# Kernel tuning notes

Measured on AMD Instinct MI355X. Metric: run time of the kernel, lower is better.

The kernel has to match this reference:

```python
import jax, jax.numpy as jnp
import numpy as np

N_HEAD = 16


def setup_inputs() -> dict:
    key = jax.random.key(0)
    ks = jax.random.split(key, 9)
    B, T, C = 4, 2048, 1024
    s = 1.0 / np.sqrt(C)
    x = jax.random.normal(ks[0], (B, T, C), dtype=jnp.float32)
    Wq = jax.random.normal(ks[1], (C, C), dtype=jnp.float32) * s
    bq = jnp.zeros((C,), dtype=jnp.float32)
    Wk = jax.random.normal(ks[2], (C, C), dtype=jnp.float32) * s
    bk = jnp.zeros((C,), dtype=jnp.float32)
    Wv = jax.random.normal(ks[3], (C, C), dtype=jnp.float32) * s
    bv = jnp.zeros((C,), dtype=jnp.float32)
    Wp = jax.random.normal(ks[4], (C, C), dtype=jnp.float32) * s
    bp = jnp.zeros((C,), dtype=jnp.float32)
    return {"x": x, "Wq": Wq, "bq": bq, "Wk": Wk, "bk": bk,
            "Wv": Wv, "bv": bv, "Wp": Wp, "bp": bp}


def reference(x, Wq, bq, Wk, bk, Wv, bv, Wp, bp):
    B, T, C = x.shape
    H = N_HEAD
    D = C // H
    # QKV projections, then split heads: [B, T, C] -> [B, H, T, D]
    def split_heads(t):
        return t.reshape(B, T, H, D).transpose(0, 2, 1, 3)
    q = split_heads(x @ Wq.T + bq)
    k = split_heads(x @ Wk.T + bk)
    v = split_heads(x @ Wv.T + bv)
    # NOTE: original code applies NO causal mask despite the class name.
    att = jnp.einsum('bhtd,bhsd->bhts', q, k) * (1.0 / jnp.sqrt(jnp.float32(D)))
    att = jax.nn.softmax(att, axis=-1)
    y = jnp.einsum('bhts,bhsd->bhtd', att, v)  # [B, H, T, D]
    y = y.transpose(0, 2, 1, 3).reshape(B, T, C)
    return y @ Wp.T + bp
```

## Files before the change

kernel.cpp:

```cpp
#include <hip/hip_runtime.h>
#include <hip/hip_bf16.h>

typedef float  f32x4   __attribute__((ext_vector_type(4)));
typedef short  bf16x8  __attribute__((ext_vector_type(8)));

__device__ __forceinline__ ushort f2b(float f) {
  union { float f; unsigned u; } x; x.f = f;
  unsigned r = x.u + 0x7fffu + ((x.u >> 16) & 1u);
  return (ushort)(r >> 16);
}

__device__ __forceinline__ unsigned pkr(float lo, float hi) {
  unsigned lu = __float_as_uint(lo) + 0x8000u;
  unsigned hu = __float_as_uint(hi) + 0x8000u;
  return __builtin_amdgcn_perm(hu, lu, 0x07060302u);
}

__device__ __forceinline__ f32x4 fzero() {
  f32x4 z; z[0] = 0.f; z[1] = 0.f; z[2] = 0.f; z[3] = 0.f; return z;
}

__device__ __forceinline__ void gld_lds16(const ushort* g, ushort* l) {
  __builtin_amdgcn_global_load_lds(g, l, 16, 0, 0);
}

__device__ __forceinline__ int vperm_s(int j64) {
  return (j64 & 0x23) | ((j64 & 0x0C) << 1) | ((j64 & 0x10) >> 2);
}

__global__ __launch_bounds__(256) void f2bf_kernel(const float* __restrict__ in,
                                                   ushort* __restrict__ out, int n4) {
  int idx = blockIdx.x * 256 + threadIdx.x;
  int stride = gridDim.x * 256;
  for (int i = idx; i < n4; i += stride) {
    float4 v = reinterpret_cast<const float4*>(in)[i];
    ushort4 o;
    o.x = f2b(v.x); o.y = f2b(v.y); o.z = f2b(v.z); o.w = f2b(v.w);
    reinterpret_cast<ushort4*>(out)[i] = o;
  }
}

__global__ __launch_bounds__(256) void f2bf_w4(
    const float* __restrict__ w0, const float* __restrict__ w1,
    const float* __restrict__ w2, const float* __restrict__ w3,
    ushort* __restrict__ out, int n4) {
  const float* src = (blockIdx.y == 0) ? w0 : (blockIdx.y == 1) ? w1
                   : (blockIdx.y == 2) ? w2 : w3;
  ushort* dst = out + (size_t)blockIdx.y * (size_t)n4 * 4;
  int idx = blockIdx.x * 256 + threadIdx.x;
  int stride = gridDim.x * 256;
  for (int i = idx; i < n4; i += stride) {
    float4 v = reinterpret_cast<const float4*>(src)[i];
    ushort4 o;
    o.x = f2b(v.x); o.y = f2b(v.y); o.z = f2b(v.z); o.w = f2b(v.w);
    reinterpret_cast<ushort4*>(dst)[i] = o;
  }
}

__global__ __launch_bounds__(256) void gemm_bt(
    const ushort* __restrict__ A, const ushort* __restrict__ B,
    const float* __restrict__ bias, float* __restrict__ Cf, ushort* __restrict__ Cb,
    int M, int N, int K, float scale) {
  __shared__ ushort As[128 * 32];
  __shared__ ushort Bs[128 * 32];
  const int tid = threadIdx.x, lane = tid & 63, wave = tid >> 6;
  const int wr = (wave >> 1) << 6, wc = (wave & 1) << 6;
  const int fr = lane & 15, fk8 = (lane >> 4) << 3;

  const size_t rowA = (size_t)blockIdx.y * 128;
  const size_t rowB = (size_t)blockIdx.x * 128;
  const ushort* Ag = A + rowA * K;
  const ushort* Bg = B + rowB * K;

  const int c0 = tid, c1 = tid + 256;
  const size_t a0 = (size_t)(c0 >> 2) * K + (size_t)((c0 & 3) << 3);
  const size_t a1 = (size_t)(c1 >> 2) * K + (size_t)((c1 & 3) << 3);

  f32x4 acc[4][4];
#pragma unroll
  for (int m = 0; m < 4; ++m)
#pragma unroll
    for (int n = 0; n < 4; ++n) acc[m][n] = fzero();

  for (int k0 = 0; k0 < K; k0 += 32) {
    __syncthreads();
    gld_lds16(Ag + a0 + k0, &As[wave * 512]);
    gld_lds16(Ag + a1 + k0, &As[2048 + wave * 512]);
    gld_lds16(Bg + a0 + k0, &Bs[wave * 512]);
    gld_lds16(Bg + a1 + k0, &Bs[2048 + wave * 512]);
    asm volatile("s_waitcnt vmcnt(0)" ::: "memory");
    __syncthreads();

    bf16x8 af[4], bfv[4];
#pragma unroll
    for (int m = 0; m < 4; ++m)
      af[m] = *reinterpret_cast<const bf16x8*>(&As[(wr + m * 16 + fr) * 32 + fk8]);
#pragma unroll
    for (int n = 0; n < 4; ++n)
      bfv[n] = *reinterpret_cast<const bf16x8*>(&Bs[(wc + n * 16 + fr) * 32 + fk8]);
#pragma unroll
    for (int m = 0; m < 4; ++m)
#pragma unroll
      for (int n = 0; n < 4; ++n)
        acc[m][n] = __builtin_amdgcn_mfma_f32_16x16x32_bf16(af[m], bfv[n], acc[m][n], 0, 0, 0);
  }

  const int orow = (lane >> 4) << 2;
#pragma unroll
  for (int m = 0; m < 4; ++m) {
#pragma unroll
    for (int n = 0; n < 4; ++n) {
      size_t gc = rowB + wc + n * 16 + fr;
      float bv = bias[gc];
#pragma unroll
      for (int r = 0; r < 4; ++r) {
        size_t gr = rowA + wr + m * 16 + orow + r;
        float v = (acc[m][n][r] + bv) * scale;
        if (Cf) Cf[gr * N + gc] = v;
        else    Cb[gr * N + gc] = f2b(v);
      }
    }
  }
}

__global__ __launch_bounds__(256) void gemm_qkv(
    const ushort* __restrict__ A, const ushort* __restrict__ Bw,
    const float* __restrict__ bq, const float* __restrict__ bk, const float* __restrict__ bv,
    ushort* __restrict__ Qb, ushort* __restrict__ Kb, ushort* __restrict__ VbT,
    float qscale) {
  __shared__ ushort As[128 * 32];
  __shared__ ushort Bs[128 * 32];
  const int tid = threadIdx.x, lane = tid & 63, wave = tid >> 6;
  const int wr = (wave >> 1) << 6, wc = (wave & 1) << 6;
  const int fr = lane & 15, fk8 = (lane >> 4) << 3;
  const int K = 1024;

  const size_t rowA = (size_t)blockIdx.y * 128;
  const size_t rowB = (size_t)blockIdx.x * 128;
  const ushort* Ag = A + rowA * K;
  const ushort* Bg = Bw + rowB * K;

  const int c0 = tid, c1 = tid + 256;
  const size_t a0 = (size_t)(c0 >> 2) * K + (size_t)((c0 & 3) << 3);
  const size_t a1 = (size_t)(c1 >> 2) * K + (size_t)((c1 & 3) << 3);

  f32x4 acc[4][4];
#pragma unroll
  for (int m = 0; m < 4; ++m)
#pragma unroll
    for (int n = 0; n < 4; ++n) acc[m][n] = fzero();

  for (int k0 = 0; k0 < K; k0 += 32) {
    __syncthreads();
    gld_lds16(Ag + a0 + k0, &As[wave * 512]);
    gld_lds16(Ag + a1 + k0, &As[2048 + wave * 512]);
    gld_lds16(Bg + a0 + k0, &Bs[wave * 512]);
    gld_lds16(Bg + a1 + k0, &Bs[2048 + wave * 512]);
    asm volatile("s_waitcnt vmcnt(0)" ::: "memory");
    __syncthreads();

    bf16x8 af[4], bfv[4];
#pragma unroll
    for (int m = 0; m < 4; ++m)
      af[m] = *reinterpret_cast<const bf16x8*>(&As[(wr + m * 16 + fr) * 32 + fk8]);
#pragma unroll
    for (int n = 0; n < 4; ++n)
      bfv[n] = *reinterpret_cast<const bf16x8*>(&Bs[(wc + n * 16 + fr) * 32 + fk8]);
#pragma unroll
    for (int m = 0; m < 4; ++m)
#pragma unroll
      for (int n = 0; n < 4; ++n)
        acc[m][n] = __builtin_amdgcn_mfma_f32_16x16x32_bf16(af[m], bfv[n], acc[m][n], 0, 0, 0);
  }

  const int stripe  = blockIdx.x >> 3;
  const int colbase = (blockIdx.x & 7) * 128;
  const int orow = (lane >> 4) << 2;
#pragma unroll
  for (int m = 0; m < 4; ++m) {
#pragma unroll
    for (int n = 0; n < 4; ++n) {
      const int gcl = colbase + wc + n * 16 + fr;
      if (stripe == 0) {
        const float bb_ = bq[gcl];
#pragma unroll
        for (int r = 0; r < 4; ++r) {
          size_t gr = rowA + wr + m * 16 + orow + r;
          Qb[gr * 1024 + gcl] = f2b((acc[m][n][r] + bb_) * qscale);
        }
      } else if (stripe == 1) {
        const float bb_ = bk[gcl];
#pragma unroll
        for (int r = 0; r < 4; ++r) {
          size_t gr = rowA + wr + m * 16 + orow + r;
          Kb[gr * 1024 + gcl] = f2b(acc[m][n][r] + bb_);
        }
      } else {
        const float bb_ = bv[gcl];
        int tt0 = (int)rowA + wr + m * 16 + orow;
        int b = tt0 >> 11, t = tt0 & 2047;
        size_t idx0 = (size_t)b * 2097152 + (size_t)gcl * 2048
                    + (size_t)((t & ~63) + vperm_s(t & 63));
        ushort4 o;
        o.x = f2b(acc[m][n][0] + bb_);
        o.y = f2b(acc[m][n][1] + bb_);
        o.z = f2b(acc[m][n][2] + bb_);
        o.w = f2b(acc[m][n][3] + bb_);
        *reinterpret_cast<ushort4*>(&VbT[idx0]) = o;
      }
    }
  }
}

__global__ __launch_bounds__(512, 2) void attn_kernel(
    const ushort* __restrict__ Qb, const ushort* __restrict__ Kb,
    const ushort* __restrict__ VbT, ushort* __restrict__ Yb) {
  __shared__ ushort lds[24576];
  const int tid = threadIdx.x, lane = tid & 63, wave = tid >> 6;
  const int fr = lane & 15, g = lane >> 4, fk8 = g << 3;
  const int bb = blockIdx.y >> 4, hh = blockIdx.y & 15;
  const size_t rowbase = (size_t)bb * 2048;
  const int cbase = hh * 64;
  const ushort* Kg  = Kb  + rowbase * 1024 + cbase;
  const ushort* VgT = VbT + (size_t)bb * 2097152 + (size_t)cbase * 2048;

  const int qbase = blockIdx.x * 256 + wave * 32;
  const ushort* qpA = &Qb[(rowbase + qbase + fr) * 1024 + cbase];
  const ushort* qpB = &Qb[(rowbase + qbase + 16 + fr) * 1024 + cbase];
  const bf16x8 qfA0 = *reinterpret_cast<const bf16x8*>(qpA + fk8);
  const bf16x8 qfA1 = *reinterpret_cast<const bf16x8*>(qpA + 32 + fk8);
  const bf16x8 qfB0 = *reinterpret_cast<const bf16x8*>(qpB + fk8);
  const bf16x8 qfB1 = *reinterpret_cast<const bf16x8*>(qpB + 32 + fk8);

  const int rS = tid >> 3;
  const int wS = (tid & 7) ^ (rS & 7);
  const ushort* sKp = Kg  + (size_t)rS * 1024 + (wS << 3);
  const ushort* sVp = VgT + (size_t)rS * 2048 + (wS << 3);
  const int wofs = wave * 512;

  const int e0 = (g ^ (fr & 7)) << 3;
  const int e1 = ((4 + g) ^ (fr & 7)) << 3;
  const ushort* lpA = &lds[fr * 64 + e0];
  const ushort* lpB = &lds[fr * 64 + e1];

  f32x4 yA[4], yB[4];
#pragma unroll
  for (int nb = 0; nb < 4; ++nb) { yA[nb] = fzero(); yB[nb] = fzero(); }
  f32x4 psA = fzero(), psB = fzero();

#define LD8(P) (*reinterpret_cast<const bf16x8*>(P))
#define MF16(A, B, C) __builtin_amdgcn_mfma_f32_16x16x32_bf16(A, B, C, 0, 0, 0)

  gld_lds16(sKp, &lds[wofs]);         gld_lds16(sVp, &lds[12288 + wofs]);   sKp += 65536; sVp += 64;
  gld_lds16(sKp, &lds[4096 + wofs]);  gld_lds16(sVp, &lds[16384 + wofs]);   sKp += 65536; sVp += 64;
  asm volatile("s_waitcnt vmcnt(2)" ::: "memory");
  __builtin_amdgcn_s_barrier();
  __builtin_amdgcn_sched_barrier(0);

#define TILE(BUF, DOPF, VMASM) do {                                              \
    if (DOPF) {                                                                  \
      gld_lds16(sKp, &lds[(((BUF) + 2) % 3) * 4096 + wofs]);                     \
      gld_lds16(sVp, &lds[12288 + (((BUF) + 2) % 3) * 4096 + wofs]);             \
      sKp += 65536; sVp += 64;                                                   \
    }                                                                            \
    f32x4 sTA[4], sTB[4];                                                        \
    _Pragma("unroll")                                                            \
    for (int jb = 0; jb < 4; ++jb) {                                             \
      bf16x8 kf0 = LD8(lpA + (BUF) * 4096 + jb * 1024);                          \
      bf16x8 kf1 = LD8(lpB + (BUF) * 4096 + jb * 1024);                          \
      f32x4 zA = fzero(), zB = fzero();                                          \
      __builtin_amdgcn_s_setprio(1);                                             \
      zA = MF16(kf0, qfA0, zA);                                                  \
      zB = MF16(kf0, qfB0, zB);                                                  \
      zA = MF16(kf1, qfA1, zA);                                                  \
      zB = MF16(kf1, qfB1, zB);                                                  \
      __builtin_amdgcn_s_setprio(0);                                             \
      sTA[jb] = zA; sTB[jb] = zB;                                                \
    }                                                                            \
    _Pragma("unroll")                                                            \
    for (int jb = 0; jb < 4; ++jb)                                               \
      _Pragma("unroll")                                                          \
      for (int r = 0; r < 4; ++r) {                                              \
        sTA[jb][r] = __builtin_exp2f(sTA[jb][r]);                                \
        sTB[jb][r] = __builtin_exp2f(sTB[jb][r]);                                \
      }                                                                          \
    _Pragma("unroll")                                                            \
    for (int r = 0; r < 4; ++r) {                                                \
      psA[r] += (sTA[0][r] + sTA[1][r]) + (sTA[2][r] + sTA[3][r]);               \
      psB[r] += (sTB[0][r] + sTB[1][r]) + (sTB[2][r] + sTB[3][r]);               \
    }                                                                            \
    union { bf16x8 v; unsigned u[4]; } paA0, paA1, paB0, paB1;                   \
    paA0.u[0] = pkr(sTA[0][0], sTA[0][1]); paA0.u[1] = pkr(sTA[0][2], sTA[0][3]);\
    paA0.u[2] = pkr(sTA[1][0], sTA[1][1]); paA0.u[3] = pkr(sTA[1][2], sTA[1][3]);\
    paA1.u[0] = pkr(sTA[2][0], sTA[2][1]); paA1.u[1] = pkr(sTA[2][2], sTA[2][3]);\
    paA1.u[2] = pkr(sTA[3][0], sTA[3][1]); paA1.u[3] = pkr(sTA[3][2], sTA[3][3]);\
    paB0.u[0] = pkr(sTB[0][0], sTB[0][1]); paB0.u[1] = pkr(sTB[0][2], sTB[0][3]);\
    paB0.u[2] = pkr(sTB[1][0], sTB[1][1]); paB0.u[3] = pkr(sTB[1][2], sTB[1][3]);\
    paB1.u[0] = pkr(sTB[2][0], sTB[2][1]); paB1.u[1] = pkr(sTB[2][2], sTB[2][3]);\
    paB1.u[2] = pkr(sTB[3][0], sTB[3][1]); paB1.u[3] = pkr(sTB[3][2], sTB[3][3]);\
    _Pragma("unroll")                                                            \
    for (int nb = 0; nb < 4; ++nb) {                                             \
      bf16x8 vf0 = LD8(lpA + 12288 + (BUF) * 4096 + nb * 1024);                  \
      bf16x8 vf1 = LD8(lpB + 12288 + (BUF) * 4096 + nb * 1024);                  \
      __builtin_amdgcn_s_setprio(1);                                             \
      yA[nb] = MF16(vf0, paA0.v, yA[nb]);                                        \
      yB[nb] = MF16(vf0, paB0.v, yB[nb]);                                        \
      yA[nb] = MF16(vf1, paA1.v, yA[nb]);                                        \
      yB[nb] = MF16(vf1, paB1.v, yB[nb]);                                        \
      __builtin_amdgcn_s_setprio(0);                                             \
    }                                                                            \
    asm volatile(VMASM ::: "memory");                                            \
    __builtin_amdgcn_s_barrier();                                                \
    __builtin_amdgcn_sched_barrier(0);                                           \
  } while (0)

  for (int tb = 0; tb < 30; tb += 3) {
    TILE(0, 1, "s_waitcnt vmcnt(2)");
    TILE(1, 1, "s_waitcnt vmcnt(2)");
    TILE(2, 1, "s_waitcnt vmcnt(2)");
  }
  TILE(0, 0, "s_waitcnt vmcnt(0)");
  TILE(1, 0, "s_waitcnt vmcnt(0)");
#undef TILE
#undef MF16
#undef LD8

  float pa_ = (psA[0] + psA[1]) + (psA[2] + psA[3]);
  pa_ += __shfl_xor(pa_, 16);
  pa_ += __shfl_xor(pa_, 32);
  float pb_ = (psB[0] + psB[1]) + (psB[2] + psB[3]);
  pb_ += __shfl_xor(pb_, 16);
  pb_ += __shfl_xor(pb_, 32);
  const float liA = 1.0f / pa_;
  const float liB = 1.0f / pb_;
  ushort* yrA = &Yb[(rowbase + qbase + fr) * 1024 + cbase];
  ushort* yrB = &Yb[(rowbase + qbase + 16 + fr) * 1024 + cbase];
#pragma unroll
  for (int nb = 0; nb < 4; ++nb) {
    ushort4 oA, oB;
    oA.x = f2b(yA[nb][0] * liA); oA.y = f2b(yA[nb][1] * liA);
    oA.z = f2b(yA[nb][2] * liA); oA.w = f2b(yA[nb][3] * liA);
    oB.x = f2b(yB[nb][0] * liB); oB.y = f2b(yB[nb][1] * liB);
    oB.z = f2b(yB[nb][2] * liB); oB.w = f2b(yB[nb][3] * liB);
    *reinterpret_cast<ushort4*>(yrA + nb * 16 + (g << 2)) = oA;
    *reinterpret_cast<ushort4*>(yrB + nb * 16 + (g << 2)) = oB;
  }
}

extern "C" void kernel_launch(void* const* d_in, const int* in_sizes, int n_in,
                              void* d_out, int out_size, void* d_ws, size_t ws_size,
                              hipStream_t stream) {
  const float* x  = (const float*)d_in[0];
  const float* Wq = (const float*)d_in[1];
  const float* bq = (const float*)d_in[2];
  const float* Wk = (const float*)d_in[3];
  const float* bk = (const float*)d_in[4];
  const float* Wv = (const float*)d_in[5];
  const float* bv = (const float*)d_in[6];
  const float* Wp = (const float*)d_in[7];
  const float* bp = (const float*)d_in[8];
  float* out = (float*)d_out;

  const int M = 8192, C = 1024;
  const size_t MC = (size_t)M * C, CC = (size_t)C * C;
  const size_t need = (MC * 5 + CC * 4) * sizeof(ushort);
  if (ws_size < need) return;

  ushort* xb  = (ushort*)d_ws;
  ushort* wqb = xb + MC;
  ushort* wpb = wqb + 3 * CC;
  ushort* Qb  = wpb + CC;
  ushort* Kb  = Qb + MC;
  ushort* VbT = Kb + MC;
  ushort* Yb  = VbT + MC;

  f2bf_kernel<<<2048, 256, 0, stream>>>(x, xb, (int)(MC / 4));
  f2bf_w4<<<dim3(256, 4), 256, 0, stream>>>(Wq, Wk, Wv, Wp, wqb, (int)(CC / 4));

  const float QSCALE = 0.18033688011112042f;
  gemm_qkv<<<dim3(24, 64), 256, 0, stream>>>(xb, wqb, bq, bk, bv, Qb, Kb, VbT, QSCALE);

  attn_kernel<<<dim3(8, 64), 512, 0, stream>>>(Qb, Kb, VbT, Yb);

  gemm_bt<<<dim3(8, 64), 256, 0, stream>>>(Yb, wpb, bp, out, nullptr, M, C, C, 1.0f);
}
```

Measured before the change: 242.6 us.

## Halve attention block size to 256 threads and use RNE packed bf16 conversion

The attention kernel now runs 256-thread blocks covering 128 queries each, launched on twice as many blocks. Each thread stages two K and two V chunks per tile, and the wait counts are adjusted to match. The aim is finer-grained scheduling and more resident blocks per CU, at the cost of loading each K/V tile twice as often overall. The probability packing also switches from a truncating add-and-permute trick to the library round-to-nearest-even float2-to-bf16 conversion, which may cost more instructions per element.

```diff
diff --git a/kernel.cpp b/kernel.cpp
--- a/kernel.cpp
+++ b/kernel.cpp
@@ -10,10 +10,9 @@
   return (ushort)(r >> 16);
 }
 
-__device__ __forceinline__ unsigned pkr(float lo, float hi) {
-  unsigned lu = __float_as_uint(lo) + 0x8000u;
-  unsigned hu = __float_as_uint(hi) + 0x8000u;
-  return __builtin_amdgcn_perm(hu, lu, 0x07060302u);
+__device__ __forceinline__ unsigned pk2(float lo, float hi) {
+  __hip_bfloat162 t = __float22bfloat162_rn(make_float2(lo, hi));
+  union { __hip_bfloat162 b; unsigned u; } c; c.b = t; return c.u;
 }
 
 __device__ __forceinline__ f32x4 fzero() {
@@ -212,7 +211,7 @@
   }
 }
 
-__global__ __launch_bounds__(512, 2) void attn_kernel(
+__global__ __launch_bounds__(256, 4) void attn_kernel(
     const ushort* __restrict__ Qb, const ushort* __restrict__ Kb,
     const ushort* __restrict__ VbT, ushort* __restrict__ Yb) {
   __shared__ ushort lds[24576];
@@ -224,7 +223,7 @@
   const ushort* Kg  = Kb  + rowbase * 1024 + cbase;
   const ushort* VgT = VbT + (size_t)bb * 2097152 + (size_t)cbase * 2048;
 
-  const int qbase = blockIdx.x * 256 + wave * 32;
+  const int qbase = blockIdx.x * 128 + wave * 32;
   const ushort* qpA = &Qb[(rowbase + qbase + fr) * 1024 + cbase];
   const ushort* qpB = &Qb[(rowbase + qbase + 16 + fr) * 1024 + cbase];
   const bf16x8 qfA0 = *reinterpret_cast<const bf16x8*>(qpA + fk8);
@@ -232,10 +231,13 @@
   const bf16x8 qfB0 = *reinterpret_cast<const bf16x8*>(qpB + fk8);
   const bf16x8 qfB1 = *reinterpret_cast<const bf16x8*>(qpB + 32 + fk8);
 
-  const int rS = tid >> 3;
-  const int wS = (tid & 7) ^ (rS & 7);
-  const ushort* sKp = Kg  + (size_t)rS * 1024 + (wS << 3);
-  const ushort* sVp = VgT + (size_t)rS * 2048 + (wS << 3);
+  const int c0 = tid, c1 = tid + 256;
+  const int r0 = c0 >> 3, r1 = c1 >> 3;
+  const int w0 = (c0 & 7) ^ (r0 & 7), w1 = (c1 & 7) ^ (r1 & 7);
+  const ushort* sK0 = Kg  + (size_t)r0 * 1024 + (w0 << 3);
+  const ushort* sK1 = Kg  + (size_t)r1 * 1024 + (w1 << 3);
+  const ushort* sV0 = VgT + (size_t)r0 * 2048 + (w0 << 3);
+  const ushort* sV1 = VgT + (size_t)r1 * 2048 + (w1 << 3);
   const int wofs = wave * 512;
 
   const int e0 = (g ^ (fr & 7)) << 3;
@@ -250,19 +252,22 @@
 
 #define LD8(P) (*reinterpret_cast<const bf16x8*>(P))
 #define MF16(A, B, C) __builtin_amdgcn_mfma_f32_16x16x32_bf16(A, B, C, 0, 0, 0)
-
-  gld_lds16(sKp, &lds[wofs]);         gld_lds16(sVp, &lds[12288 + wofs]);   sKp += 65536; sVp += 64;
-  gld_lds16(sKp, &lds[4096 + wofs]);  gld_lds16(sVp, &lds[16384 + wofs]);   sKp += 65536; sVp += 64;
-  asm volatile("s_waitcnt vmcnt(2)" ::: "memory");
+#define STAGE(BUF) do {                                                          \
+    gld_lds16(sK0, &lds[(BUF) * 4096 + wofs]);                                   \
+    gld_lds16(sK1, &lds[(BUF) * 4096 + 2048 + wofs]);                            \
+    gld_lds16(sV0, &lds[12288 + (BUF) * 4096 + wofs]);                           \
+    gld_lds16(sV1, &lds[12288 + (BUF) * 4096 + 2048 + wofs]);                    \
+    sK0 += 65536; sK1 += 65536; sV0 += 64; sV1 += 64;                            \
+  } while (0)
+
+  STAGE(0);
+  STAGE(1);
+  asm volatile("s_waitcnt vmcnt(4)" ::: "memory");
   __builtin_amdgcn_s_barrier();
   __builtin_amdgcn_sched_barrier(0);
 
 #define TILE(BUF, DOPF, VMASM) do {                                              \
-    if (DOPF) {                                                                  \
-      gld_lds16(sKp, &lds[(((BUF) + 2) % 3) * 4096 + wofs]);                     \
-      gld_lds16(sVp, &lds[12288 + (((BUF) + 2) % 3) * 4096 + wofs]);             \
-      sKp += 65536; sVp += 64;                                                   \
-    }                                                                            \
+    if (DOPF) STAGE(((BUF) + 2) % 3);                                            \
     f32x4 sTA[4], sTB[4];                                                        \
     _Pragma("unroll")                                                            \
     for (int jb = 0; jb < 4; ++jb) {                                             \
@@ -290,14 +295,14 @@
       psB[r] += (sTB[0][r] + sTB[1][r]) + (sTB[2][r] + sTB[3][r]);               \
     }                                                                            \
     union { bf16x8 v; unsigned u[4]; } paA0, paA1, paB0, paB1;                   \
-    paA0.u[0] = pkr(sTA[0][0], sTA[0][1]); paA0.u[1] = pkr(sTA[0][2], sTA[0][3]);\
-    paA0.u[2] = pkr(sTA[1][0], sTA[1][1]); paA0.u[3] = pkr(sTA[1][2], sTA[1][3]);\
-    paA1.u[0] = pkr(sTA[2][0], sTA[2][1]); paA1.u[1] = pkr(sTA[2][2], sTA[2][3]);\
-    paA1.u[2] = pkr(sTA[3][0], sTA[3][1]); paA1.u[3] = pkr(sTA[3][2], sTA[3][3]);\
-    paB0.u[0] = pkr(sTB[0][0], sTB[0][1]); paB0.u[1] = pkr(sTB[0][2], sTB[0][3]);\
-    paB0.u[2] = pkr(sTB[1][0], sTB[1][1]); paB0.u[3] = pkr(sTB[1][2], sTB[1][3]);\
-    paB1.u[0] = pkr(sTB[2][0], sTB[2][1]); paB1.u[1] = pkr(sTB[2][2], sTB[2][3]);\
-    paB1.u[2] = pkr(sTB[3][0], sTB[3][1]); paB1.u[3] = pkr(sTB[3][2], sTB[3][3]);\
+    paA0.u[0] = pk2(sTA[0][0], sTA[0][1]); paA0.u[1] = pk2(sTA[0][2], sTA[0][3]);\
+    paA0.u[2] = pk2(sTA[1][0], sTA[1][1]); paA0.u[3] = pk2(sTA[1][2], sTA[1][3]);\
+    paA1.u[0] = pk2(sTA[2][0], sTA[2][1]); paA1.u[1] = pk2(sTA[2][2], sTA[2][3]);\
+    paA1.u[2] = pk2(sTA[3][0], sTA[3][1]); paA1.u[3] = pk2(sTA[3][2], sTA[3][3]);\
+    paB0.u[0] = pk2(sTB[0][0], sTB[0][1]); paB0.u[1] = pk2(sTB[0][2], sTB[0][3]);\
+    paB0.u[2] = pk2(sTB[1][0], sTB[1][1]); paB0.u[3] = pk2(sTB[1][2], sTB[1][3]);\
+    paB1.u[0] = pk2(sTB[2][0], sTB[2][1]); paB1.u[1] = pk2(sTB[2][2], sTB[2][3]);\
+    paB1.u[2] = pk2(sTB[3][0], sTB[3][1]); paB1.u[3] = pk2(sTB[3][2], sTB[3][3]);\
     _Pragma("unroll")                                                            \
     for (int nb = 0; nb < 4; ++nb) {                                             \
       bf16x8 vf0 = LD8(lpA + 12288 + (BUF) * 4096 + nb * 1024);                  \
@@ -315,13 +320,14 @@
   } while (0)
 
   for (int tb = 0; tb < 30; tb += 3) {
-    TILE(0, 1, "s_waitcnt vmcnt(2)");
-    TILE(1, 1, "s_waitcnt vmcnt(2)");
-    TILE(2, 1, "s_waitcnt vmcnt(2)");
+    TILE(0, 1, "s_waitcnt vmcnt(4)");
+    TILE(1, 1, "s_waitcnt vmcnt(4)");
+    TILE(2, 1, "s_waitcnt vmcnt(4)");
   }
   TILE(0, 0, "s_waitcnt vmcnt(0)");
   TILE(1, 0, "s_waitcnt vmcnt(0)");
 #undef TILE
+#undef STAGE
 #undef MF16
 #undef LD8
 
@@ -380,7 +386,7 @@
   const float QSCALE = 0.18033688011112042f;
   gemm_qkv<<<dim3(24, 64), 256, 0, stream>>>(xb, wqb, bq, bk, bv, Qb, Kb, VbT, QSCALE);
 
-  attn_kernel<<<dim3(8, 64), 512, 0, stream>>>(Qb, Kb, VbT, Yb);
+  attn_kernel<<<dim3(16, 64), 256, 0, stream>>>(Qb, Kb, VbT, Yb);
 
   gemm_bt<<<dim3(8, 64), 256, 0, stream>>>(Yb, wpb, bp, out, nullptr, M, C, C, 1.0f);
 }
```

Result: slower. 250.5 us (+3.3%).
